# Performance work log

Measured on AMD Instinct MI355X. Metric: run time of the kernel, lower is better.

The kernel has to match this reference:

```python
import jax, jax.numpy as jnp
import numpy as np

EPS = 1e-6
OHEM_RATIO = 3
NUM_KERNELS = 6
ALPHA = 0.5


def _dice_loss(inp, tgt, mask):
    # inp/tgt/mask: [B, H, W] -> scalar mean over batch
    B = inp.shape[0]
    i = (inp * mask).reshape(B, -1)
    t = (tgt * mask).reshape(B, -1)
    inter = jnp.sum(i * t, axis=1)
    union = jnp.sum(i * i, axis=1) + jnp.sum(t * t, axis=1) + EPS
    return jnp.mean(1.0 - 2.0 * inter / union)


def _ohem_mask(pred_prob, gt, tmask, ratio=OHEM_RATIO):
    # Vectorized per-sample OHEM: keep all positives plus the top
    # min(ratio*n_pos, n_neg) highest-scoring negatives.
    B, H, W = pred_prob.shape
    p = pred_prob.reshape(B, -1)
    g = gt.reshape(B, -1)
    m = tmask.reshape(B, -1)
    pos = (g > 0.5) & (m > 0.5)
    neg = (g <= 0.5) & (m > 0.5)
    n_pos = jnp.sum(pos, axis=1)
    n_neg = jnp.minimum(ratio * n_pos, jnp.sum(neg, axis=1))  # [B]
    scores = jnp.where(neg, p, -jnp.inf)
    # descending rank of each pixel's score within its sample
    order = jnp.argsort(-scores, axis=1)
    rank = jnp.argsort(order, axis=1)
    hard_neg = neg & (rank < n_neg[:, None])
    return (pos | hard_neg).astype(jnp.float32).reshape(B, H, W)


def setup_inputs() -> dict:
    key = jax.random.key(0)
    k1, k2, k3, k4 = jax.random.split(key, 4)
    B, C, H, W = 16, 6, 640, 640
    pred = jax.random.normal(k1, (B, C, H, W), dtype=jnp.float32)
    gt_text = (jax.random.uniform(k2, (B, 1, H, W)) > 0.9).astype(jnp.float32)
    gt_kernels = (jax.random.uniform(k3, (B, C - 1, H, W)) > 0.9).astype(jnp.float32)
    training_mask = (jax.random.uniform(k4, (B, 1, H, W)) > 0.05).astype(jnp.float32)
    return {"pred": pred, "gt_text": gt_text, "gt_kernels": gt_kernels,
            "training_mask": training_mask}


def reference(pred, gt_text, gt_kernels, training_mask):
    pred_text = pred[:, 0, :, :]                 # [B,H,W]
    pred_kernels = pred[:, 1:, :, :]             # [B,K,H,W]
    gt_text = gt_text[:, 0, :, :]                # squeeze(1)
    tmask = training_mask[:, 0, :, :]

    # original computes sigmoid + OHEM under no_grad -> stop_gradient
    pred_prob = jax.lax.stop_gradient(jax.nn.sigmoid(pred_text))
    ohem = jax.lax.stop_gradient(_ohem_mask(pred_prob, gt_text, tmask))

    loss_text = _dice_loss(pred_prob, gt_text, ohem)

    # vectorized dice over the K=num_kernels-1 kernel maps, mask broadcast
    pk = jax.nn.sigmoid(pred_kernels)            # [B,K,H,W]
    m = tmask[:, None, :, :]
    i = pk * m
    t = gt_kernels * m
    inter = jnp.sum(i * t, axis=(2, 3))          # [B,K]
    union = jnp.sum(i * i, axis=(2, 3)) + jnp.sum(t * t, axis=(2, 3)) + EPS
    # mean over kernels of (mean over batch) == mean over (B,K)
    loss_kernels = jnp.mean(1.0 - 2.0 * inter / union)

    loss = loss_kernels + ALPHA * loss_text
    return (loss, loss_text, loss_kernels)
```

## Files before the change

### kernel.cpp

```cpp
#include <hip/hip_runtime.h>
#include <math.h>

#define HW 409600
#define BB 16
#define CPRED 6
#define NKER 5
#define NBINS 1024
#define CHUNKS 128
#define EPSF 1e-6f

__device__ __forceinline__ float sigmoidf_(float x) {
    return __builtin_amdgcn_rcpf(1.0f + __expf(-x));
}

__global__ __launch_bounds__(256, 8) void pass1_kernel(
    const float* __restrict__ pred, const float* __restrict__ gt_text,
    const float* __restrict__ gt_k, const float* __restrict__ tmask,
    float* __restrict__ hist_cnt, float* __restrict__ hist_p2,
    float* __restrict__ bstats, float* __restrict__ kstats)
{
    __shared__ float s_cnt[NBINS + 1];
    __shared__ float s_p2[NBINS + 1];
    __shared__ float s_red[19][4];

    const int b = blockIdx.y;
    const int chunk = blockIdx.x;
    const int tid = threadIdx.x;

    for (int i = tid; i <= NBINS; i += 256) { s_cnt[i] = 0.f; s_p2[i] = 0.f; }
    __syncthreads();

    const int NV4 = HW / 4;
    const float4* tm4 = reinterpret_cast<const float4*>(tmask + (size_t)b * HW);
    const float4* gt4 = reinterpret_cast<const float4*>(gt_text + (size_t)b * HW);
    const float4* pt4 = reinterpret_cast<const float4*>(pred + (size_t)b * CPRED * HW);
    const float4* gk4 = reinterpret_cast<const float4*>(gt_k + (size_t)b * NKER * HW);

    const int per = NV4 / CHUNKS;
    const int i0 = chunk * per;
    const int i1 = i0 + per;

    float n_pos = 0.f, n_neg = 0.f, sp = 0.f, sp2 = 0.f;
    float kin[NKER], kui[NKER], kut[NKER];
    #pragma unroll
    for (int c = 0; c < NKER; ++c) { kin[c] = 0.f; kui[c] = 0.f; kut[c] = 0.f; }

    for (int i = i0 + tid; i < i1; i += 256) {
        float4 m4  = tm4[i];
        float4 g4  = gt4[i];
        float4 x4  = pt4[i];
        float4 xk0 = pt4[(size_t)1 * NV4 + i];
        float4 xk1 = pt4[(size_t)2 * NV4 + i];
        float4 xk2 = pt4[(size_t)3 * NV4 + i];
        float4 xk3 = pt4[(size_t)4 * NV4 + i];
        float4 xk4 = pt4[(size_t)5 * NV4 + i];
        float4 gg0 = gk4[(size_t)0 * NV4 + i];
        float4 gg1 = gk4[(size_t)1 * NV4 + i];
        float4 gg2 = gk4[(size_t)2 * NV4 + i];
        float4 gg3 = gk4[(size_t)3 * NV4 + i];
        float4 gg4 = gk4[(size_t)4 * NV4 + i];

        #define TEXT1(mm, xx, ggt) { \
            float p = sigmoidf_(xx); \
            float posf = (mm) * (ggt); \
            float negf = (mm) - posf; \
            float pp_ = p * p; \
            n_pos += posf; n_neg += negf; \
            sp += posf * p; sp2 += posf * pp_; \
            int bin = (int)(p * (float)NBINS); \
            bin = bin > NBINS - 1 ? NBINS - 1 : bin; \
            bin = negf > 0.f ? bin : NBINS; \
            atomicAdd(&s_cnt[bin], 1.f); \
            atomicAdd(&s_p2[bin], pp_); \
        }
        TEXT1(m4.x, x4.x, g4.x)
        TEXT1(m4.y, x4.y, g4.y)
        TEXT1(m4.z, x4.z, g4.z)
        TEXT1(m4.w, x4.w, g4.w)
        #undef TEXT1

        #define KCH(c, xk, gg) { \
            float p0 = sigmoidf_(xk.x), p1 = sigmoidf_(xk.y); \
            float p2_ = sigmoidf_(xk.z), p3 = sigmoidf_(xk.w); \
            kin[c] += m4.x * p0 * gg.x + m4.y * p1 * gg.y \
                    + m4.z * p2_ * gg.z + m4.w * p3 * gg.w; \
            kui[c] += m4.x * p0 * p0 + m4.y * p1 * p1 \
                    + m4.z * p2_ * p2_ + m4.w * p3 * p3; \
            kut[c] += m4.x * gg.x + m4.y * gg.y + m4.z * gg.z + m4.w * gg.w; \
        }
        KCH(0, xk0, gg0)
        KCH(1, xk1, gg1)
        KCH(2, xk2, gg2)
        KCH(3, xk3, gg3)
        KCH(4, xk4, gg4)
        #undef KCH
    }

    const int lane = tid & 63;
    const int wv = tid >> 6;
    #define WRED(v) { for (int o_ = 32; o_ > 0; o_ >>= 1) v += __shfl_down(v, o_, 64); }
    WRED(n_pos) WRED(n_neg) WRED(sp) WRED(sp2)
    if (lane == 0) {
        s_red[0][wv] = n_pos; s_red[1][wv] = n_neg;
        s_red[2][wv] = sp;    s_red[3][wv] = sp2;
    }
    #pragma unroll
    for (int c = 0; c < NKER; ++c) {
        float a = kin[c], u = kui[c], t = kut[c];
        WRED(a) WRED(u) WRED(t)
        if (lane == 0) {
            s_red[4 + c * 3 + 0][wv] = a;
            s_red[4 + c * 3 + 1][wv] = u;
            s_red[4 + c * 3 + 2][wv] = t;
        }
    }
    #undef WRED
    __syncthreads();

    if (tid < 19) {
        float a = s_red[tid][0] + s_red[tid][1] + s_red[tid][2] + s_red[tid][3];
        float* dst;
        if (tid < 4) dst = &bstats[b * 4 + tid];
        else {
            int q = tid - 4;
            dst = &kstats[(b * NKER + q / 3) * 3 + (q % 3)];
        }
        atomicAdd(dst, a);
    }

    for (int i = tid; i < NBINS; i += 256) {
        float c = s_cnt[i];
        if (c != 0.f) {
            atomicAdd(&hist_cnt[b * NBINS + i], c);
            atomicAdd(&hist_p2[b * NBINS + i], s_p2[i]);
        }
    }
}

__global__ __launch_bounds__(64) void finalize_batch_kernel(
    const float* __restrict__ hist_cnt, const float* __restrict__ hist_p2,
    const float* __restrict__ bstats, const float* __restrict__ kstats,
    float* __restrict__ btext, float* __restrict__ bkterm)
{
    const int b = blockIdx.x;
    const int lane = threadIdx.x;
    const int SEG = NBINS / 64;

    float cg = 0.f, pg = 0.f;
    {
        int base = b * NBINS + lane * SEG;
        #pragma unroll
        for (int k = 0; k < SEG; ++k) {
            cg += hist_cnt[base + k];
            pg += hist_p2[base + k];
        }
    }
    float pc = cg, pp = pg;
    #pragma unroll
    for (int o = 1; o < 64; o <<= 1) {
        float tc = __shfl_up(pc, o, 64);
        float tp = __shfl_up(pp, o, 64);
        if (lane >= o) { pc += tc; pp += tp; }
    }
    float totc = __shfl(pc, 63, 64);
    float totp = __shfl(pp, 63, 64);
    float sufc = totc - pc;
    float sufp = totp - pp;

    float n_pos  = bstats[b * 4 + 0];
    float n_negt = bstats[b * 4 + 1];
    float sp     = bstats[b * 4 + 2];
    float sp2    = bstats[b * 4 + 3];
    float n_sel  = fminf(3.0f * n_pos, n_negt);

    float hard_p2 = 0.f;
    bool cross = (sufc < n_sel) && (sufc + cg >= n_sel);
    unsigned long long bal = __ballot(cross);
    if (n_sel <= 0.f) {
        hard_p2 = 0.f;
    } else if (bal == 0ULL) {
        hard_p2 = totp;
    } else {
        int ls = 63 - __builtin_clzll(bal);
        float run  = __shfl(sufc, ls, 64);
        float runp = __shfl(sufp, ls, 64);
        float bc = 0.f, bp = 0.f;
        if (lane < SEG) {
            int idx = b * NBINS + ls * SEG + lane;
            bc = hist_cnt[idx];
            bp = hist_p2[idx];
        }
        float pc2 = bc, pp2 = bp;
        #pragma unroll
        for (int o = 1; o < 64; o <<= 1) {
            float tc = __shfl_up(pc2, o, 64);
            float tp = __shfl_up(pp2, o, 64);
            if (lane >= o) { pc2 += tc; pp2 += tp; }
        }
        float tot2c = __shfl(pc2, SEG - 1, 64);
        float tot2p = __shfl(pp2, SEG - 1, 64);
        float suf2c = tot2c - pc2;
        float suf2p = tot2p - pp2;
        bool cross2 = (lane < SEG) && (run + suf2c < n_sel) && (run + suf2c + bc >= n_sel);
        unsigned long long bal2 = __ballot(cross2);
        if (bal2 == 0ULL) {
            hard_p2 = runp + tot2p;
        } else {
            int ks = 63 - __builtin_clzll(bal2);
            float rs  = __shfl(suf2c, ks, 64);
            float rsp = __shfl(suf2p, ks, 64);
            float cc  = __shfl(bc, ks, 64);
            float cp  = __shfl(bp, ks, 64);
            float need = n_sel - (run + rs);
            hard_p2 = runp + rsp + (cc > 0.f ? cp * (need / cc) : 0.f);
        }
    }

    if (lane == 0) {
        float uni = sp2 + n_pos + hard_p2 + EPSF;
        btext[b] = 1.0f - 2.0f * sp / uni;
    }
    if (lane < NKER) {
        int idx = b * NKER + lane;
        float a = kstats[idx * 3 + 0];
        float u = kstats[idx * 3 + 1];
        float t = kstats[idx * 3 + 2];
        bkterm[idx] = 1.0f - 2.0f * a / (u + t + EPSF);
    }
}

__global__ __launch_bounds__(64) void combine_kernel(
    const float* __restrict__ btext, const float* __restrict__ bkterm,
    float* __restrict__ out)
{
    const int lane = threadIdx.x;
    float t = (lane < BB) ? btext[lane] : 0.f;
    float k = bkterm[lane];
    if (lane < BB * NKER - 64) k += bkterm[64 + lane];
    #define WRED(v) { for (int o_ = 32; o_ > 0; o_ >>= 1) v += __shfl_down(v, o_, 64); }
    WRED(t) WRED(k)
    #undef WRED
    if (lane == 0) {
        float lt = t / (float)BB;
        float lk = k / (float)(BB * NKER);
        out[0] = lk + 0.5f * lt;
        out[1] = lt;
        out[2] = lk;
    }
}

extern "C" void kernel_launch(void* const* d_in, const int* in_sizes, int n_in,
                              void* d_out, int out_size, void* d_ws, size_t ws_size,
                              hipStream_t stream)
{
    const float* pred    = (const float*)d_in[0];
    const float* gt_text = (const float*)d_in[1];
    const float* gt_k    = (const float*)d_in[2];
    const float* tmask   = (const float*)d_in[3];

    float* ws = (float*)d_ws;
    float* hist_cnt = ws;
    float* hist_p2  = ws + (size_t)BB * NBINS;
    float* bstats   = ws + (size_t)2 * BB * NBINS;
    float* kstats   = bstats + BB * 4;
    float* btext    = kstats + BB * NKER * 3;
    float* bkterm   = btext + BB;

    size_t zero_bytes = ((size_t)2 * BB * NBINS + BB * 4 + BB * NKER * 3) * sizeof(float);
    hipMemsetAsync(d_ws, 0, zero_bytes, stream);

    dim3 grid(CHUNKS, BB), block(256);
    hipLaunchKernelGGL(pass1_kernel, grid, block, 0, stream,
                       pred, gt_text, gt_k, tmask, hist_cnt, hist_p2, bstats, kstats);
    hipLaunchKernelGGL(finalize_batch_kernel, dim3(BB), dim3(64), 0, stream,
                       hist_cnt, hist_p2, bstats, kstats, btext, bkterm);
    hipLaunchKernelGGL(combine_kernel, dim3(1), dim3(64), 0, stream,
                       btext, bkterm, (float*)d_out);
}
```

Before: 372.9 us.

## Software-pipeline pass1 loads with double-buffered registers and branch out non-negative histogram atomics

```diff
diff --git a/kernel.cpp b/kernel.cpp
--- a/kernel.cpp
+++ b/kernel.cpp
@@ -6,28 +6,34 @@
 #define CPRED 6
 #define NKER 5
 #define NBINS 1024
-#define CHUNKS 128
+#define CHUNKS 100
 #define EPSF 1e-6f
 
 __device__ __forceinline__ float sigmoidf_(float x) {
     return __builtin_amdgcn_rcpf(1.0f + __expf(-x));
 }
 
-__global__ __launch_bounds__(256, 8) void pass1_kernel(
+struct Pix {
+    float4 m, g, x;
+    float4 xk0, xk1, xk2, xk3, xk4;
+    float4 gg0, gg1, gg2, gg3, gg4;
+};
+
+__global__ __launch_bounds__(256, 3) void pass1_kernel(
     const float* __restrict__ pred, const float* __restrict__ gt_text,
     const float* __restrict__ gt_k, const float* __restrict__ tmask,
     float* __restrict__ hist_cnt, float* __restrict__ hist_p2,
     float* __restrict__ bstats, float* __restrict__ kstats)
 {
-    __shared__ float s_cnt[NBINS + 1];
-    __shared__ float s_p2[NBINS + 1];
+    __shared__ float s_cnt[NBINS];
+    __shared__ float s_p2[NBINS];
     __shared__ float s_red[19][4];
 
     const int b = blockIdx.y;
     const int chunk = blockIdx.x;
     const int tid = threadIdx.x;
 
-    for (int i = tid; i <= NBINS; i += 256) { s_cnt[i] = 0.f; s_p2[i] = 0.f; }
+    for (int i = tid; i < NBINS; i += 256) { s_cnt[i] = 0.f; s_p2[i] = 0.f; }
     __syncthreads();
 
     const int NV4 = HW / 4;
@@ -37,67 +43,85 @@
     const float4* gk4 = reinterpret_cast<const float4*>(gt_k + (size_t)b * NKER * HW);
 
     const int per = NV4 / CHUNKS;
-    const int i0 = chunk * per;
-    const int i1 = i0 + per;
+    const int base = chunk * per + tid;
 
     float n_pos = 0.f, n_neg = 0.f, sp = 0.f, sp2 = 0.f;
-    float kin[NKER], kui[NKER], kut[NKER];
-    #pragma unroll
-    for (int c = 0; c < NKER; ++c) { kin[c] = 0.f; kui[c] = 0.f; kut[c] = 0.f; }
-
-    for (int i = i0 + tid; i < i1; i += 256) {
-        float4 m4  = tm4[i];
-        float4 g4  = gt4[i];
-        float4 x4  = pt4[i];
-        float4 xk0 = pt4[(size_t)1 * NV4 + i];
-        float4 xk1 = pt4[(size_t)2 * NV4 + i];
-        float4 xk2 = pt4[(size_t)3 * NV4 + i];
-        float4 xk3 = pt4[(size_t)4 * NV4 + i];
-        float4 xk4 = pt4[(size_t)5 * NV4 + i];
-        float4 gg0 = gk4[(size_t)0 * NV4 + i];
-        float4 gg1 = gk4[(size_t)1 * NV4 + i];
-        float4 gg2 = gk4[(size_t)2 * NV4 + i];
-        float4 gg3 = gk4[(size_t)3 * NV4 + i];
-        float4 gg4 = gk4[(size_t)4 * NV4 + i];
-
-        #define TEXT1(mm, xx, ggt) { \
-            float p = sigmoidf_(xx); \
-            float posf = (mm) * (ggt); \
-            float negf = (mm) - posf; \
-            float pp_ = p * p; \
-            n_pos += posf; n_neg += negf; \
-            sp += posf * p; sp2 += posf * pp_; \
+    float kin0 = 0.f, kin1 = 0.f, kin2 = 0.f, kin3 = 0.f, kin4 = 0.f;
+    float kui0 = 0.f, kui1 = 0.f, kui2 = 0.f, kui3 = 0.f, kui4 = 0.f;
+    float kut0 = 0.f, kut1 = 0.f, kut2 = 0.f, kut3 = 0.f, kut4 = 0.f;
+
+    #define LOADP(P, idx) { \
+        int i_ = (idx); \
+        P.m   = tm4[i_]; \
+        P.g   = gt4[i_]; \
+        P.x   = pt4[i_]; \
+        P.xk0 = pt4[(size_t)1 * NV4 + i_]; \
+        P.gg0 = gk4[(size_t)0 * NV4 + i_]; \
+        P.xk1 = pt4[(size_t)2 * NV4 + i_]; \
+        P.gg1 = gk4[(size_t)1 * NV4 + i_]; \
+        P.xk2 = pt4[(size_t)3 * NV4 + i_]; \
+        P.gg2 = gk4[(size_t)2 * NV4 + i_]; \
+        P.xk3 = pt4[(size_t)4 * NV4 + i_]; \
+        P.gg3 = gk4[(size_t)3 * NV4 + i_]; \
+        P.xk4 = pt4[(size_t)5 * NV4 + i_]; \
+        P.gg4 = gk4[(size_t)4 * NV4 + i_]; \
+    }
+
+    #define TEXT1(mm, xx, ggt) { \
+        float p = sigmoidf_(xx); \
+        float posf = (mm) * (ggt); \
+        float negf = (mm) - posf; \
+        n_pos += posf; n_neg += negf; \
+        sp += posf * p; sp2 += posf * p * p; \
+        if (negf > 0.f) { \
             int bin = (int)(p * (float)NBINS); \
             bin = bin > NBINS - 1 ? NBINS - 1 : bin; \
-            bin = negf > 0.f ? bin : NBINS; \
             atomicAdd(&s_cnt[bin], 1.f); \
-            atomicAdd(&s_p2[bin], pp_); \
-        }
-        TEXT1(m4.x, x4.x, g4.x)
-        TEXT1(m4.y, x4.y, g4.y)
-        TEXT1(m4.z, x4.z, g4.z)
-        TEXT1(m4.w, x4.w, g4.w)
-        #undef TEXT1
-
-        #define KCH(c, xk, gg) { \
-            float p0 = sigmoidf_(xk.x), p1 = sigmoidf_(xk.y); \
-            float p2_ = sigmoidf_(xk.z), p3 = sigmoidf_(xk.w); \
-            kin[c] += m4.x * p0 * gg.x + m4.y * p1 * gg.y \
-                    + m4.z * p2_ * gg.z + m4.w * p3 * gg.w; \
-            kui[c] += m4.x * p0 * p0 + m4.y * p1 * p1 \
-                    + m4.z * p2_ * p2_ + m4.w * p3 * p3; \
-            kut[c] += m4.x * gg.x + m4.y * gg.y + m4.z * gg.z + m4.w * gg.w; \
-        }
-        KCH(0, xk0, gg0)
-        KCH(1, xk1, gg1)
-        KCH(2, xk2, gg2)
-        KCH(3, xk3, gg3)
-        KCH(4, xk4, gg4)
-        #undef KCH
-    }
+            atomicAdd(&s_p2[bin], p * p); \
+        } \
+    }
+
+    #define KCH(P, kin, kui, kut, xkf, ggf) { \
+        float p0 = sigmoidf_(P.xkf.x), p1 = sigmoidf_(P.xkf.y); \
+        float p2_ = sigmoidf_(P.xkf.z), p3 = sigmoidf_(P.xkf.w); \
+        kin += P.m.x * p0 * P.ggf.x + P.m.y * p1 * P.ggf.y \
+             + P.m.z * p2_ * P.ggf.z + P.m.w * p3 * P.ggf.w; \
+        kui += P.m.x * p0 * p0 + P.m.y * p1 * p1 \
+             + P.m.z * p2_ * p2_ + P.m.w * p3 * p3; \
+        kut += P.m.x * P.ggf.x + P.m.y * P.ggf.y \
+             + P.m.z * P.ggf.z + P.m.w * P.ggf.w; \
+    }
+
+    #define PROC(P) { \
+        TEXT1(P.m.x, P.x.x, P.g.x) \
+        TEXT1(P.m.y, P.x.y, P.g.y) \
+        TEXT1(P.m.z, P.x.z, P.g.z) \
+        TEXT1(P.m.w, P.x.w, P.g.w) \
+        KCH(P, kin0, kui0, kut0, xk0, gg0) \
+        KCH(P, kin1, kui1, kut1, xk1, gg1) \
+        KCH(P, kin2, kui2, kut2, xk2, gg2) \
+        KCH(P, kin3, kui3, kut3, xk3, gg3) \
+        KCH(P, kin4, kui4, kut4, xk4, gg4) \
+    }
+
+    Pix A, B;
+    LOADP(A, base)
+    #pragma unroll
+    for (int k = 0; k < 4; ++k) {
+        if (k < 3) LOADP(B, base + (k + 1) * 256)
+        PROC(A)
+        if (k < 3) A = B;
+    }
+    #undef LOADP
+    #undef TEXT1
+    #undef KCH
+    #undef PROC
 
     const int lane = tid & 63;
     const int wv = tid >> 6;
+    float kin[NKER] = {kin0, kin1, kin2, kin3, kin4};
+    float kui[NKER] = {kui0, kui1, kui2, kui3, kui4};
+    float kut[NKER] = {kut0, kut1, kut2, kut3, kut4};
     #define WRED(v) { for (int o_ = 32; o_ > 0; o_ >>= 1) v += __shfl_down(v, o_, 64); }
     WRED(n_pos) WRED(n_neg) WRED(sp) WRED(sp2)
     if (lane == 0) {
```

Result: slower. 405.9 us (+8.8%).

## Double-buffer tiles into LDS via async global_load_lds with fewer persistent blocks

Applied to the files above, without the earlier changes.

```diff
diff --git a/kernel.cpp b/kernel.cpp
--- a/kernel.cpp
+++ b/kernel.cpp
@@ -6,98 +6,136 @@
 #define CPRED 6
 #define NKER 5
 #define NBINS 1024
-#define CHUNKS 128
 #define EPSF 1e-6f
+
+#define HW4 (HW / 4)
+#define TILE4 256
+#define NCH 13
+#define CHELEM (NCH * TILE4)
+#define SEGS 16
+#define TILES_PER_SEG 25
 
 __device__ __forceinline__ float sigmoidf_(float x) {
     return __builtin_amdgcn_rcpf(1.0f + __expf(-x));
 }
 
-__global__ __launch_bounds__(256, 8) void pass1_kernel(
+__global__ __launch_bounds__(256) void pass1_kernel(
     const float* __restrict__ pred, const float* __restrict__ gt_text,
     const float* __restrict__ gt_k, const float* __restrict__ tmask,
     float* __restrict__ hist_cnt, float* __restrict__ hist_p2,
     float* __restrict__ bstats, float* __restrict__ kstats)
 {
-    __shared__ float s_cnt[NBINS + 1];
-    __shared__ float s_p2[NBINS + 1];
+    __shared__ float4 sbuf[2 * CHELEM];
+    __shared__ float s_cnt[NBINS];
+    __shared__ float s_p2[NBINS];
     __shared__ float s_red[19][4];
 
+    const int seg = blockIdx.x;
     const int b = blockIdx.y;
-    const int chunk = blockIdx.x;
     const int tid = threadIdx.x;
-
-    for (int i = tid; i <= NBINS; i += 256) { s_cnt[i] = 0.f; s_p2[i] = 0.f; }
+    const int lane = tid & 63;
+    const int wv = tid >> 6;
+
+    for (int i = tid; i < NBINS; i += 256) { s_cnt[i] = 0.f; s_p2[i] = 0.f; }
     __syncthreads();
 
-    const int NV4 = HW / 4;
-    const float4* tm4 = reinterpret_cast<const float4*>(tmask + (size_t)b * HW);
-    const float4* gt4 = reinterpret_cast<const float4*>(gt_text + (size_t)b * HW);
-    const float4* pt4 = reinterpret_cast<const float4*>(pred + (size_t)b * CPRED * HW);
-    const float4* gk4 = reinterpret_cast<const float4*>(gt_k + (size_t)b * NKER * HW);
-
-    const int per = NV4 / CHUNKS;
-    const int i0 = chunk * per;
-    const int i1 = i0 + per;
+    const float4* P  = reinterpret_cast<const float4*>(pred)    + (size_t)b * CPRED * HW4;
+    const float4* GT = reinterpret_cast<const float4*>(gt_text) + (size_t)b * HW4;
+    const float4* GK = reinterpret_cast<const float4*>(gt_k)    + (size_t)b * NKER * HW4;
+    const float4* TM = reinterpret_cast<const float4*>(tmask)   + (size_t)b * HW4;
+
+    #define STG(c, bp) { \
+        const float4* ga_ = (bp) + (size_t)t_ * TILE4 + wv * 64 + lane; \
+        __builtin_amdgcn_global_load_lds( \
+            (const __attribute__((address_space(1))) void*)ga_, \
+            (__attribute__((address_space(3))) void*)&sbuf[nb_ * CHELEM + (c) * TILE4 + wv * 64], \
+            16, 0, 0); \
+    }
+    #define STAGE_ALL(nbv, tv) { \
+        const int nb_ = (nbv); const int t_ = (tv); \
+        STG(0, P) STG(1, P + HW4) STG(2, P + 2 * HW4) \
+        STG(3, P + 3 * HW4) STG(4, P + 4 * HW4) STG(5, P + 5 * HW4) \
+        STG(6, GT) \
+        STG(7, GK) STG(8, GK + HW4) STG(9, GK + 2 * HW4) \
+        STG(10, GK + 3 * HW4) STG(11, GK + 4 * HW4) \
+        STG(12, TM) \
+    }
 
     float n_pos = 0.f, n_neg = 0.f, sp = 0.f, sp2 = 0.f;
-    float kin[NKER], kui[NKER], kut[NKER];
-    #pragma unroll
-    for (int c = 0; c < NKER; ++c) { kin[c] = 0.f; kui[c] = 0.f; kut[c] = 0.f; }
-
-    for (int i = i0 + tid; i < i1; i += 256) {
-        float4 m4  = tm4[i];
-        float4 g4  = gt4[i];
-        float4 x4  = pt4[i];
-        float4 xk0 = pt4[(size_t)1 * NV4 + i];
-        float4 xk1 = pt4[(size_t)2 * NV4 + i];
-        float4 xk2 = pt4[(size_t)3 * NV4 + i];
-        float4 xk3 = pt4[(size_t)4 * NV4 + i];
-        float4 xk4 = pt4[(size_t)5 * NV4 + i];
-        float4 gg0 = gk4[(size_t)0 * NV4 + i];
-        float4 gg1 = gk4[(size_t)1 * NV4 + i];
-        float4 gg2 = gk4[(size_t)2 * NV4 + i];
-        float4 gg3 = gk4[(size_t)3 * NV4 + i];
-        float4 gg4 = gk4[(size_t)4 * NV4 + i];
-
-        #define TEXT1(mm, xx, ggt) { \
-            float p = sigmoidf_(xx); \
-            float posf = (mm) * (ggt); \
-            float negf = (mm) - posf; \
-            float pp_ = p * p; \
-            n_pos += posf; n_neg += negf; \
-            sp += posf * p; sp2 += posf * pp_; \
+    float kin0 = 0.f, kin1 = 0.f, kin2 = 0.f, kin3 = 0.f, kin4 = 0.f;
+    float kui0 = 0.f, kui1 = 0.f, kui2 = 0.f, kui3 = 0.f, kui4 = 0.f;
+    float kut0 = 0.f, kut1 = 0.f, kut2 = 0.f, kut3 = 0.f, kut4 = 0.f;
+
+    #define TEXT1(mm, xx, ggt) { \
+        float p = sigmoidf_(xx); \
+        float posf = (mm) * (ggt); \
+        float negf = (mm) - posf; \
+        n_pos += posf; n_neg += negf; \
+        sp += posf * p; sp2 += posf * p * p; \
+        if (negf > 0.f) { \
             int bin = (int)(p * (float)NBINS); \
             bin = bin > NBINS - 1 ? NBINS - 1 : bin; \
-            bin = negf > 0.f ? bin : NBINS; \
             atomicAdd(&s_cnt[bin], 1.f); \
-            atomicAdd(&s_p2[bin], pp_); \
-        }
+            atomicAdd(&s_p2[bin], p * p); \
+        } \
+    }
+    #define KCH(xk, gg, kin, kui, kut) { \
+        float p0 = sigmoidf_(xk.x), p1 = sigmoidf_(xk.y); \
+        float p2_ = sigmoidf_(xk.z), p3 = sigmoidf_(xk.w); \
+        kin += m4.x * p0 * gg.x + m4.y * p1 * gg.y \
+             + m4.z * p2_ * gg.z + m4.w * p3 * gg.w; \
+        kui += m4.x * p0 * p0 + m4.y * p1 * p1 \
+             + m4.z * p2_ * p2_ + m4.w * p3 * p3; \
+        kut += m4.x * gg.x + m4.y * gg.y + m4.z * gg.z + m4.w * gg.w; \
+    }
+
+    const int t0 = seg * TILES_PER_SEG;
+    STAGE_ALL(0, t0)
+
+    for (int k = 0; k < TILES_PER_SEG; ++k) {
+        const int cur = k & 1;
+        if (k < TILES_PER_SEG - 1) {
+            STAGE_ALL(cur ^ 1, t0 + k + 1)
+            asm volatile("s_waitcnt vmcnt(13)" ::: "memory");
+        } else {
+            asm volatile("s_waitcnt vmcnt(0)" ::: "memory");
+        }
+        __builtin_amdgcn_sched_barrier(0);
+
+        const int o = cur * CHELEM + tid;
+        float4 x4  = sbuf[o + 0 * TILE4];
+        float4 xk0 = sbuf[o + 1 * TILE4];
+        float4 xk1 = sbuf[o + 2 * TILE4];
+        float4 xk2 = sbuf[o + 3 * TILE4];
+        float4 xk3 = sbuf[o + 4 * TILE4];
+        float4 xk4 = sbuf[o + 5 * TILE4];
+        float4 g4  = sbuf[o + 6 * TILE4];
+        float4 gg0 = sbuf[o + 7 * TILE4];
+        float4 gg1 = sbuf[o + 8 * TILE4];
+        float4 gg2 = sbuf[o + 9 * TILE4];
+        float4 gg3 = sbuf[o + 10 * TILE4];
+        float4 gg4 = sbuf[o + 11 * TILE4];
+        float4 m4  = sbuf[o + 12 * TILE4];
+
         TEXT1(m4.x, x4.x, g4.x)
         TEXT1(m4.y, x4.y, g4.y)
         TEXT1(m4.z, x4.z, g4.z)
         TEXT1(m4.w, x4.w, g4.w)
-        #undef TEXT1
-
-        #define KCH(c, xk, gg) { \
-            float p0 = sigmoidf_(xk.x), p1 = sigmoidf_(xk.y); \
-            float p2_ = sigmoidf_(xk.z), p3 = sigmoidf_(xk.w); \
-            kin[c] += m4.x * p0 * gg.x + m4.y * p1 * gg.y \
-                    + m4.z * p2_ * gg.z + m4.w * p3 * gg.w; \
-            kui[c] += m4.x * p0 * p0 + m4.y * p1 * p1 \
-                    + m4.z * p2_ * p2_ + m4.w * p3 * p3; \
-            kut[c] += m4.x * gg.x + m4.y * gg.y + m4.z * gg.z + m4.w * gg.w; \
-        }
-        KCH(0, xk0, gg0)
-        KCH(1, xk1, gg1)
-        KCH(2, xk2, gg2)
-        KCH(3, xk3, gg3)
-        KCH(4, xk4, gg4)
-        #undef KCH
-    }
-
-    const int lane = tid & 63;
-    const int wv = tid >> 6;
+        KCH(xk0, gg0, kin0, kui0, kut0)
+        KCH(xk1, gg1, kin1, kui1, kut1)
+        KCH(xk2, gg2, kin2, kui2, kut2)
+        KCH(xk3, gg3, kin3, kui3, kut3)
+        KCH(xk4, gg4, kin4, kui4, kut4)
+        __builtin_amdgcn_sched_barrier(0);
+    }
+    #undef STG
+    #undef STAGE_ALL
+    #undef TEXT1
+    #undef KCH
+
+    float kin[NKER] = {kin0, kin1, kin2, kin3, kin4};
+    float kui[NKER] = {kui0, kui1, kui2, kui3, kui4};
+    float kut[NKER] = {kut0, kut1, kut2, kut3, kut4};
     #define WRED(v) { for (int o_ = 32; o_ > 0; o_ >>= 1) v += __shfl_down(v, o_, 64); }
     WRED(n_pos) WRED(n_neg) WRED(sp) WRED(sp2)
     if (lane == 0) {
@@ -269,7 +307,7 @@
     size_t zero_bytes = ((size_t)2 * BB * NBINS + BB * 4 + BB * NKER * 3) * sizeof(float);
     hipMemsetAsync(d_ws, 0, zero_bytes, stream);
 
-    dim3 grid(CHUNKS, BB), block(256);
+    dim3 grid(SEGS, BB), block(256);
     hipLaunchKernelGGL(pass1_kernel, grid, block, 0, stream,
                        pred, gt_text, gt_k, tmask, hist_cnt, hist_p2, bstats, kstats);
     hipLaunchKernelGGL(finalize_batch_kernel, dim3(BB), dim3(64), 0, stream,
```

Result: faster. 361.6 us (-3.0%).
